# Performance work log

Measured on AMD Instinct MI355X. Metric: run time of the kernel, lower is better.

## Reference

```python
import jax, jax.numpy as jnp
import numpy as np

B, L, D = 4, 8192, 512


def setup_inputs() -> dict:
    key = jax.random.key(0)
    kx, kwg, kwc = jax.random.split(key, 3)
    x = jax.random.normal(kx, (B, L, D), dtype=jnp.float32)
    # Xavier-uniform init for DxD linears
    bound = float(np.sqrt(6.0 / (D + D)))
    Wg = jax.random.uniform(kwg, (D, D), minval=-bound, maxval=bound, dtype=jnp.float32)
    bg = jnp.ones((D,), dtype=jnp.float32)   # gate bias init to 1.0
    Wc = jax.random.uniform(kwc, (D, D), minval=-bound, maxval=bound, dtype=jnp.float32)
    bc = jnp.zeros((D,), dtype=jnp.float32)
    return {"x": x, "Wg": Wg, "bg": bg, "Wc": Wc, "bc": bc}


def _mingru_scan(gates, cands):
    # h_t = (1 - g_t) * h_{t-1} + g_t * c_t, h_0 = 0
    # linear recurrence h_t = a_t h_{t-1} + b_t with a = 1-g, b = g*c
    a = 1.0 - gates
    b = gates * cands

    def combine(left, right):
        a_l, b_l = left
        a_r, b_r = right
        return a_r * a_l, a_r * b_l + b_r

    _, h = jax.lax.associative_scan(combine, (a, b), axis=1)
    return h


def reference(x, Wg, bg, Wc, bc):
    gates = jax.nn.sigmoid(jnp.einsum('bld,ed->ble', x, Wg) + bg)
    cands = jnp.tanh(jnp.einsum('bld,ed->ble', x, Wc) + bc)
    return _mingru_scan(gates, cands)
```

## Files before the change

### kernel.cpp

```cpp
#include <hip/hip_runtime.h>
#include <stdint.h>
#include <stddef.h>

#define B_ 4
#define L_ 8192
#define D_ 512
#define M_ (B_*L_)
#define K_ 512
#define CHUNK 64
#define NC (L_/CHUNK)

typedef _Float16 f16;
typedef f16 f16x2 __attribute__((ext_vector_type(2)));
typedef f16 f16x4 __attribute__((ext_vector_type(4)));
typedef f16 f16x8 __attribute__((ext_vector_type(8)));
typedef float f32x4 __attribute__((ext_vector_type(4)));

__device__ __forceinline__ void async16(const void* g, void* l) {
  __builtin_amdgcn_global_load_lds(
      (const __attribute__((address_space(1))) uint32_t*)g,
      (__attribute__((address_space(3))) uint32_t*)l,
      16, 0, 0);
}

__global__ __launch_bounds__(256) void prep_w(const float* __restrict__ Wg,
                                              const float* __restrict__ Wc,
                                              f16* __restrict__ wp) {
  const int idx = (blockIdx.x * 256 + threadIdx.x) * 4;
  const float* src = (idx < 262144) ? (Wg + idx) : (Wc + (idx - 262144));
  float4 v = *(const float4*)src;
  f16x4 o = {(f16)v.x, (f16)v.y, (f16)v.z, (f16)v.w};
  *(f16x4*)(wp + idx) = o;
}

__global__ __launch_bounds__(256, 2) void gemm_act(
    const float* __restrict__ X, const f16* __restrict__ Wp,
    const float* __restrict__ bg, const float* __restrict__ bc,
    uint32_t* __restrict__ AC,
    float* __restrict__ cA, float* __restrict__ cB) {
  __shared__ __align__(16) f16 sA[2][128 * 32];
  __shared__ __align__(16) f16 sBg[2][128 * 32];
  __shared__ __align__(16) f16 sBc[2][128 * 32];

  const int tid = threadIdx.x;
  const int id = blockIdx.x;
  const int xcd = id & 7;
  const int slot = id >> 3;
  const int g_ = xcd * 128 + slot;
  const int bm = g_ >> 2;
  const int bn = g_ & 3;

  const int lane = tid & 63;
  const int w = tid >> 6;
  const int wm = w >> 1, wn = w & 1;
  const int l15 = lane & 15, quad = lane >> 4;

  const int srow = tid >> 2;
  const int spc8 = (tid & 3) * 8;
  const float* gx = X + (size_t)(bm * 128 + srow) * K_ + spc8;
  const f16* gBg = Wp + (size_t)(bn * 128 + srow) * K_ + spc8;
  const f16* gBc = Wp + (size_t)(512 + bn * 128 + srow) * K_ + spc8;

  f32x4 accG[4][4] = {};
  f32x4 accC[4][4] = {};

  float4 ax0, ax1, ax2, ax3;

#define ISSUE(kk, bN) \
    ax0 = *(const float4*)(gx + (kk)); \
    ax1 = *(const float4*)(gx + (kk) + 4); \
    ax2 = *(const float4*)(gx + 64 * K_ + (kk)); \
    ax3 = *(const float4*)(gx + 64 * K_ + (kk) + 4); \
    async16(gBg + (kk), &sBg[bN][tid * 8]); \
    async16(gBg + 64 * K_ + (kk), &sBg[bN][tid * 8 + 64 * 32]); \
    async16(gBc + (kk), &sBc[bN][tid * 8]); \
    async16(gBc + 64 * K_ + (kk), &sBc[bN][tid * 8 + 64 * 32]);

#define BODY(kt, bC, bN, DO_ISSUE) { \
    asm volatile("s_waitcnt vmcnt(0)" ::: "memory"); \
    f16x8 w0 = {(f16)ax0.x, (f16)ax0.y, (f16)ax0.z, (f16)ax0.w, \
                (f16)ax1.x, (f16)ax1.y, (f16)ax1.z, (f16)ax1.w}; \
    f16x8 w1 = {(f16)ax2.x, (f16)ax2.y, (f16)ax2.z, (f16)ax2.w, \
                (f16)ax3.x, (f16)ax3.y, (f16)ax3.z, (f16)ax3.w}; \
    *(f16x8*)&sA[bC][tid * 8] = w0; \
    *(f16x8*)&sA[bC][tid * 8 + 64 * 32] = w1; \
    if (DO_ISSUE) { ISSUE((kt + 1) * 32, bN); } \
    asm volatile("s_waitcnt lgkmcnt(0)" ::: "memory"); \
    __builtin_amdgcn_s_barrier(); \
    f16x8 af[4], bgf[4], bcf[4]; \
    _Pragma("unroll") \
    for (int i = 0; i < 4; i++) \
      af[i] = *(const f16x8*)(&sA[bC][(wm * 64 + i * 16 + l15) * 32 + quad * 8]); \
    _Pragma("unroll") \
    for (int j = 0; j < 4; j++) { \
      bgf[j] = *(const f16x8*)(&sBg[bC][(wn * 64 + j * 16 + l15) * 32 + quad * 8]); \
      bcf[j] = *(const f16x8*)(&sBc[bC][(wn * 64 + j * 16 + l15) * 32 + quad * 8]); \
    } \
    _Pragma("unroll") \
    for (int i = 0; i < 4; i++) \
      _Pragma("unroll") \
      for (int j = 0; j < 4; j++) { \
        accG[i][j] = __builtin_amdgcn_mfma_f32_16x16x32_f16(af[i], bgf[j], accG[i][j], 0, 0, 0); \
        accC[i][j] = __builtin_amdgcn_mfma_f32_16x16x32_f16(af[i], bcf[j], accC[i][j], 0, 0, 0); \
      } \
    __builtin_amdgcn_sched_barrier(0); \
    __builtin_amdgcn_s_barrier(); \
  }

  ISSUE(0, 0);
  for (int kt2 = 0; kt2 < 7; kt2++) {
    const int kt = kt2 * 2;
    BODY(kt,     0, 1, 1);
    BODY(kt + 1, 1, 0, 1);
  }
  BODY(14, 0, 1, 1);
  BODY(15, 1, 0, 0);
#undef BODY
#undef ISSUE

  const int c = bm * 2 + wm;
#pragma unroll
  for (int j = 0; j < 4; j++) {
    const int col = bn * 128 + wn * 64 + j * 16 + l15;
    const float bgv = bg[col];
    const float bcv = bc[col];
    float blkP[4], blkQ[4];
#pragma unroll
    for (int i = 0; i < 4; i++) {
      const int mrow = bm * 128 + wm * 64 + i * 16 + quad * 4;
      float P = 1.0f, Q = 0.0f;
#pragma unroll
      for (int r = 0; r < 4; r++) {
        float yg = accG[i][j][r] + bgv;
        float gg = 1.0f / (1.0f + __expf(-yg));
        float yc = accC[i][j][r] + bcv;
        yc = fminf(fmaxf(yc, -15.0f), 15.0f);
        float t = __expf(2.0f * yc);
        float cc = (t - 1.0f) / (t + 1.0f);
        f16x2 p;
        p[0] = (f16)(1.0f - gg);
        p[1] = (f16)(gg * cc);
        *(f16x2*)&AC[(size_t)(mrow + r) * 512 + col] = p;
        const float av = (float)p[0];
        const float bv = (float)p[1];
        Q = fmaf(av, Q, bv);
        P *= av;
      }
      float Pp = __shfl_xor(P, 16);
      float Qp = __shfl_xor(Q, 16);
      float nP = P * Pp;
      float nQ = (quad & 1) ? fmaf(P, Qp, Q) : fmaf(Pp, Q, Qp);
      Pp = __shfl_xor(nP, 32);
      Qp = __shfl_xor(nQ, 32);
      blkP[i] = nP * Pp;
      blkQ[i] = (quad & 2) ? fmaf(nP, Qp, nQ) : fmaf(Pp, nQ, Qp);
    }
    float CP = blkP[0], CQ = blkQ[0];
#pragma unroll
    for (int i = 1; i < 4; i++) {
      CQ = fmaf(blkP[i], CQ, blkQ[i]);
      CP *= blkP[i];
    }
    if (quad == 0) {
      cA[(size_t)c * 512 + col] = CP;
      cB[(size_t)c * 512 + col] = CQ;
    }
  }
}

__global__ __launch_bounds__(256) void scan_apply(
    const uint32_t* __restrict__ AC,
    const float* __restrict__ cA, const float* __restrict__ cB,
    float* __restrict__ out) {
  const int blk = blockIdx.x;
  const int ch = blk & (NC - 1);
  const int bseq = blk >> 7;
  const int d0 = threadIdx.x * 2;

  float h0 = 0.0f, h1 = 0.0f;
  const float* pA = cA + (size_t)(bseq * NC) * 512 + d0;
  const float* pB = cB + (size_t)(bseq * NC) * 512 + d0;
#pragma unroll 4
  for (int cc = 0; cc < ch; cc++) {
    float2 va = *(const float2*)(pA + (size_t)cc * 512);
    float2 vb = *(const float2*)(pB + (size_t)cc * 512);
    h0 = fmaf(va.x, h0, vb.x);
    h1 = fmaf(va.y, h1, vb.y);
  }

  const size_t base = (size_t)blk * CHUNK * 512 + d0;
#pragma unroll 8
  for (int t = 0; t < CHUNK; t++) {
    const size_t i = base + (size_t)t * 512;
    uint2 v = *(const uint2*)&AC[i];
    f16x2 p0 = __builtin_bit_cast(f16x2, v.x);
    f16x2 p1 = __builtin_bit_cast(f16x2, v.y);
    h0 = fmaf((float)p0[0], h0, (float)p0[1]);
    h1 = fmaf((float)p1[0], h1, (float)p1[1]);
    float2 o;
    o.x = h0;
    o.y = h1;
    *(float2*)&out[i] = o;
  }
}

extern "C" void kernel_launch(void* const* d_in, const int* in_sizes, int n_in,
                              void* d_out, int out_size, void* d_ws, size_t ws_size,
                              hipStream_t stream) {
  const float* x  = (const float*)d_in[0];
  const float* Wg = (const float*)d_in[1];
  const float* bg = (const float*)d_in[2];
  const float* Wc = (const float*)d_in[3];
  const float* bc = (const float*)d_in[4];
  float* out = (float*)d_out;

  char* ws = (char*)d_ws;
  f16*      wp = (f16*)(ws);
  uint32_t* AC = (uint32_t*)(ws + 1048576);
  float*    cA = (float*)(ws + 69206016);
  float*    cB = (float*)(ws + 70254592);

  prep_w<<<512, 256, 0, stream>>>(Wg, Wc, wp);
  gemm_act<<<(M_ / 128) * 4, 256, 0, stream>>>(x, wp, bg, bc, AC, cA, cB);
  scan_apply<<<B_ * NC, 256, 0, stream>>>(AC, cA, cB, out);
}
```

Measured before the change: 211.3 us.

## Deepen GEMM prefetch pipeline and move chunk-prefix scan into separate kernel

Result: slower. 219.3 us (+3.8%).

```diff
diff --git a/kernel.cpp b/kernel.cpp
--- a/kernel.cpp
+++ b/kernel.cpp
@@ -66,27 +66,27 @@
 
   float4 ax0, ax1, ax2, ax3;
 
-#define ISSUE(kk, bN) \
+#define ISSUE_A(kk) { \
     ax0 = *(const float4*)(gx + (kk)); \
     ax1 = *(const float4*)(gx + (kk) + 4); \
     ax2 = *(const float4*)(gx + 64 * K_ + (kk)); \
-    ax3 = *(const float4*)(gx + 64 * K_ + (kk) + 4); \
+    ax3 = *(const float4*)(gx + 64 * K_ + (kk) + 4); }
+
+#define STAGE_B(kk, bN) { \
     async16(gBg + (kk), &sBg[bN][tid * 8]); \
     async16(gBg + 64 * K_ + (kk), &sBg[bN][tid * 8 + 64 * 32]); \
     async16(gBc + (kk), &sBc[bN][tid * 8]); \
-    async16(gBc + 64 * K_ + (kk), &sBc[bN][tid * 8 + 64 * 32]);
-
-#define BODY(kt, bC, bN, DO_ISSUE) { \
-    asm volatile("s_waitcnt vmcnt(0)" ::: "memory"); \
+    async16(gBc + 64 * K_ + (kk), &sBc[bN][tid * 8 + 64 * 32]); }
+
+#define WRITE_A(bN) { \
     f16x8 w0 = {(f16)ax0.x, (f16)ax0.y, (f16)ax0.z, (f16)ax0.w, \
                 (f16)ax1.x, (f16)ax1.y, (f16)ax1.z, (f16)ax1.w}; \
     f16x8 w1 = {(f16)ax2.x, (f16)ax2.y, (f16)ax2.z, (f16)ax2.w, \
                 (f16)ax3.x, (f16)ax3.y, (f16)ax3.z, (f16)ax3.w}; \
-    *(f16x8*)&sA[bC][tid * 8] = w0; \
-    *(f16x8*)&sA[bC][tid * 8 + 64 * 32] = w1; \
-    if (DO_ISSUE) { ISSUE((kt + 1) * 32, bN); } \
-    asm volatile("s_waitcnt lgkmcnt(0)" ::: "memory"); \
-    __builtin_amdgcn_s_barrier(); \
+    *(f16x8*)&sA[bN][tid * 8] = w0; \
+    *(f16x8*)&sA[bN][tid * 8 + 64 * 32] = w1; }
+
+#define COMPUTE(bC) { \
     f16x8 af[4], bgf[4], bcf[4]; \
     _Pragma("unroll") \
     for (int i = 0; i < 4; i++) \
@@ -102,21 +102,37 @@
       for (int j = 0; j < 4; j++) { \
         accG[i][j] = __builtin_amdgcn_mfma_f32_16x16x32_f16(af[i], bgf[j], accG[i][j], 0, 0, 0); \
         accC[i][j] = __builtin_amdgcn_mfma_f32_16x16x32_f16(af[i], bcf[j], accC[i][j], 0, 0, 0); \
-      } \
-    __builtin_amdgcn_sched_barrier(0); \
-    __builtin_amdgcn_s_barrier(); \
-  }
-
-  ISSUE(0, 0);
-  for (int kt2 = 0; kt2 < 7; kt2++) {
-    const int kt = kt2 * 2;
-    BODY(kt,     0, 1, 1);
-    BODY(kt + 1, 1, 0, 1);
-  }
-  BODY(14, 0, 1, 1);
-  BODY(15, 1, 0, 0);
+      } }
+
+  ISSUE_A(0);
+  STAGE_B(0, 0);
+  WRITE_A(0);
+  asm volatile("" ::: "memory");
+  ISSUE_A(32);
+  asm volatile("s_waitcnt vmcnt(4) lgkmcnt(0)" ::: "memory");
+  __builtin_amdgcn_s_barrier();
+
+#define BODY(kt, bC, bN, DO_ISSUE) { \
+    STAGE_B(((kt) + 1) * 32, bN); \
+    WRITE_A(bN); \
+    asm volatile("" ::: "memory"); \
+    if (DO_ISSUE) { ISSUE_A(((kt) + 2) * 32); } \
+    COMPUTE(bC); \
+    if (DO_ISSUE) { asm volatile("s_waitcnt vmcnt(4) lgkmcnt(0)" ::: "memory"); } \
+    else          { asm volatile("s_waitcnt vmcnt(0) lgkmcnt(0)" ::: "memory"); } \
+    __builtin_amdgcn_s_barrier(); }
+
+  for (int t2 = 0; t2 < 7; t2++) {
+    BODY(t2 * 2,     0, 1, 1);
+    BODY(t2 * 2 + 1, 1, 0, 1);
+  }
+  BODY(14, 0, 1, 0);
+  COMPUTE(1);
 #undef BODY
-#undef ISSUE
+#undef COMPUTE
+#undef WRITE_A
+#undef STAGE_B
+#undef ISSUE_A
 
   const int c = bm * 2 + wm;
 #pragma unroll
@@ -168,26 +184,26 @@
   }
 }
 
+__global__ __launch_bounds__(64) void scan_chunks(
+    const float* __restrict__ cA, const float* __restrict__ cB,
+    float* __restrict__ Hpre) {
+  const int b = blockIdx.x >> 3;
+  const int d = ((blockIdx.x & 7) << 6) + threadIdx.x;
+  float h = 0.0f;
+#pragma unroll 8
+  for (int ch = 0; ch < NC; ch++) {
+    const int idx = (b * NC + ch) * 512 + d;
+    Hpre[idx] = h;
+    h = fmaf(cA[idx], h, cB[idx]);
+  }
+}
+
 __global__ __launch_bounds__(256) void scan_apply(
-    const uint32_t* __restrict__ AC,
-    const float* __restrict__ cA, const float* __restrict__ cB,
+    const uint32_t* __restrict__ AC, const float* __restrict__ Hpre,
     float* __restrict__ out) {
   const int blk = blockIdx.x;
-  const int ch = blk & (NC - 1);
-  const int bseq = blk >> 7;
   const int d0 = threadIdx.x * 2;
-
-  float h0 = 0.0f, h1 = 0.0f;
-  const float* pA = cA + (size_t)(bseq * NC) * 512 + d0;
-  const float* pB = cB + (size_t)(bseq * NC) * 512 + d0;
-#pragma unroll 4
-  for (int cc = 0; cc < ch; cc++) {
-    float2 va = *(const float2*)(pA + (size_t)cc * 512);
-    float2 vb = *(const float2*)(pB + (size_t)cc * 512);
-    h0 = fmaf(va.x, h0, vb.x);
-    h1 = fmaf(va.y, h1, vb.y);
-  }
-
+  float2 h = *(const float2*)&Hpre[blk * 512 + d0];
   const size_t base = (size_t)blk * CHUNK * 512 + d0;
 #pragma unroll 8
   for (int t = 0; t < CHUNK; t++) {
@@ -195,12 +211,9 @@
     uint2 v = *(const uint2*)&AC[i];
     f16x2 p0 = __builtin_bit_cast(f16x2, v.x);
     f16x2 p1 = __builtin_bit_cast(f16x2, v.y);
-    h0 = fmaf((float)p0[0], h0, (float)p0[1]);
-    h1 = fmaf((float)p1[0], h1, (float)p1[1]);
-    float2 o;
-    o.x = h0;
-    o.y = h1;
-    *(float2*)&out[i] = o;
+    h.x = fmaf((float)p0[0], h.x, (float)p0[1]);
+    h.y = fmaf((float)p1[0], h.y, (float)p1[1]);
+    *(float2*)&out[i] = h;
   }
 }
 
@@ -217,10 +230,12 @@
   char* ws = (char*)d_ws;
   f16*      wp = (f16*)(ws);
   uint32_t* AC = (uint32_t*)(ws + 1048576);
-  float*    cA = (float*)(ws + 69206016);
-  float*    cB = (float*)(ws + 70254592);
+  float*    cA = (float*)(ws + 68157440);
+  float*    cB = (float*)(ws + 69206016);
+  float*    Hp = (float*)(ws + 70254592);
 
   prep_w<<<512, 256, 0, stream>>>(Wg, Wc, wp);
   gemm_act<<<(M_ / 128) * 4, 256, 0, stream>>>(x, wp, bg, bc, AC, cA, cB);
-  scan_apply<<<B_ * NC, 256, 0, stream>>>(AC, cA, cB, out);
-}
+  scan_chunks<<<32, 64, 0, stream>>>(cA, cB, Hp);
+  scan_apply<<<B_ * NC, 256, 0, stream>>>(AC, Hp, out);
+}
```
